# Optimization experiments

Measured on AMD Instinct MI355X. Metric: run time of the kernel, lower is better.

## Reference

```python
import jax, jax.numpy as jnp
import numpy as np


def _gru_layer(x_seq, W_ih, W_hh, b_ih, b_hh):
    # x_seq: [B, T, D_in]; PyTorch gate order: r, z, n
    B, T, _ = x_seq.shape
    H = W_hh.shape[1]
    # Precompute input-to-hidden gates for all timesteps (one big GEMM)
    gx = jnp.einsum('btd,gd->btg', x_seq, W_ih) + b_ih  # [B, T, 3H]

    def step(h, gx_t):
        gh = h @ W_hh.T + b_hh  # [B, 3H]
        r = jax.nn.sigmoid(gx_t[:, :H] + gh[:, :H])
        z = jax.nn.sigmoid(gx_t[:, H:2 * H] + gh[:, H:2 * H])
        n = jnp.tanh(gx_t[:, 2 * H:] + r * gh[:, 2 * H:])
        h_new = (1.0 - z) * n + z * h
        return h_new, h_new

    h0 = jnp.zeros((B, H), dtype=x_seq.dtype)
    _, hs = jax.lax.scan(step, h0, jnp.swapaxes(gx, 0, 1))  # hs: [T, B, H]
    return jnp.swapaxes(hs, 0, 1)  # [B, T, H]


def setup_inputs() -> dict:
    key = jax.random.key(0)
    ks = jax.random.split(key, 11)
    B, T, D, H, O = 64, 512, 128, 512, 1
    s_ih0 = 1.0 / np.sqrt(D)
    s_h = 1.0 / np.sqrt(H)
    return {
        'X': jax.random.normal(ks[0], (B, T, D), dtype=jnp.float32),
        'W_ih0': jax.random.normal(ks[1], (3 * H, D), dtype=jnp.float32) * s_ih0,
        'W_hh0': jax.random.normal(ks[2], (3 * H, H), dtype=jnp.float32) * s_h,
        'b_ih0': jax.random.normal(ks[3], (3 * H,), dtype=jnp.float32) * s_h,
        'b_hh0': jax.random.normal(ks[4], (3 * H,), dtype=jnp.float32) * s_h,
        'W_ih1': jax.random.normal(ks[5], (3 * H, H), dtype=jnp.float32) * s_h,
        'W_hh1': jax.random.normal(ks[6], (3 * H, H), dtype=jnp.float32) * s_h,
        'b_ih1': jax.random.normal(ks[7], (3 * H,), dtype=jnp.float32) * s_h,
        'b_hh1': jax.random.normal(ks[8], (3 * H,), dtype=jnp.float32) * s_h,
        'W_fc': jax.random.normal(ks[9], (O, H), dtype=jnp.float32) * s_h,
        'b_fc': jax.random.normal(ks[10], (O,), dtype=jnp.float32) * s_h,
    }


def reference(X, W_ih0, W_hh0, b_ih0, b_hh0, W_ih1, W_hh1, b_ih1, b_hh1, W_fc, b_fc):
    h1 = _gru_layer(X, W_ih0, W_hh0, b_ih0, b_hh0)     # [B, T, H]
    h2 = _gru_layer(h1, W_ih1, W_hh1, b_ih1, b_hh1)    # [B, T, H]
    out = h2[:, -1, :] @ W_fc.T + b_fc                 # [B, O]
    return out
```

## Files before the change

kernel.cpp:

```cpp
#include <hip/hip_runtime.h>
#include <math.h>

#define B_  64
#define T_  512
#define D0_ 128
#define H_  512
#define G3_ 1536
#define HSTR 512
#define BSTR 528
#define BKg 32
#define SENT 0x7FC00000u

typedef short short8 __attribute__((ext_vector_type(8)));
typedef float f32x4 __attribute__((ext_vector_type(4)));
typedef unsigned uint32x4 __attribute__((ext_vector_type(4)));

__device__ __forceinline__ float fast_sig(float x) {
  return __builtin_amdgcn_rcpf(1.f + __expf(-x));
}
__device__ __forceinline__ float fast_tanh(float x) {
  return 1.f - 2.f * __builtin_amdgcn_rcpf(1.f + __expf(2.f * x));
}

__device__ __forceinline__ unsigned short f2bf_rne(float f) {
  unsigned u = __float_as_uint(f);
  unsigned r = (u + 0x7fffu + ((u >> 16) & 1u)) >> 16;
  return (unsigned short)r;
}
__device__ __forceinline__ float bf2f(unsigned short h) {
  return __uint_as_float(((unsigned)h) << 16);
}

__global__ __launch_bounds__(768, 3) void scan_kernel(
    const unsigned short* __restrict__ WhH, const unsigned short* __restrict__ WhL,
    const float* __restrict__ bhh,
    const float* __restrict__ gx, float* __restrict__ hist,
    int t0, int tc, int gxt0, int gxT)
{
  __shared__ float hsh[4 * HSTR];
  __shared__ unsigned short hbh[4 * BSTR];
  __shared__ unsigned short hbl[4 * BSTR];
  __shared__ float ghp[2][96 * 5];
  __shared__ float bsh[96];

  const int tid = threadIdx.x;
  const int blk = blockIdx.x;
  const int g = blk >> 4, c = blk & 15;
  const int j0 = c << 5;
  const int bbase = g << 2;

  const int wv = tid >> 6, lane = tid & 63;
  const int mtile = wv >> 1, half = wv & 1;
  const int rloc = lane & 15, kq = lane >> 4;
  const int row = mtile * 16 + rloc;
  const int wrow = (row >> 5) * H_ + j0 + (row & 31);

  short8 wh[8], wl[8];
  {
    const unsigned short* RH = WhH + (size_t)wrow * H_ + half * 256 + (kq << 3);
    const unsigned short* RL = WhL + (size_t)wrow * H_ + half * 256 + (kq << 3);
    #pragma unroll
    for (int cc = 0; cc < 8; ++cc) {
      wh[cc] = *(const short8*)(RH + cc * 32);
      wl[cc] = *(const short8*)(RL + cc * 32);
    }
  }
  if (tid < 96)
    bsh[tid] = bhh[(tid >> 5) * H_ + j0 + (tid & 31)];

  size_t go0 = 0;
  if (tid < 128) {
    int bb = tid >> 5, j = tid & 31;
    go0 = ((size_t)(bbase + bb) * gxT) * (size_t)G3_ + j0 + j;
  }
  __syncthreads();

  for (int t = t0; t < t0 + tc; ++t) {
    if (t == 0) {
      for (int idx = tid; idx < 2048; idx += 768) hsh[idx] = 0.f;
      for (int idx = tid; idx < 4 * BSTR; idx += 768) {
        hbh[idx] = 0; hbl[idx] = 0;
      }
    } else if (tid < 512) {
      const int bb = tid >> 7, e4 = tid & 127;
      const unsigned* qp = (const unsigned*)
          (hist + ((size_t)(bbase + bb) * T_ + (t - 1)) * H_) + (e4 << 2);
      uint32x4 v;
      for (;;) {
        asm volatile(
            "global_load_dwordx4 %0, %1, off sc0 sc1\n\t"
            "s_waitcnt vmcnt(0)"
            : "=&v"(v) : "v"(qp) : "memory");
        if (v.x != SENT && v.y != SENT && v.z != SENT && v.w != SENT) break;
      }
      float4 f = make_float4(__uint_as_float(v.x), __uint_as_float(v.y),
                             __uint_as_float(v.z), __uint_as_float(v.w));
      *(float4*)&hsh[bb * HSTR + (e4 << 2)] = f;
      unsigned short h0 = f2bf_rne(f.x), h1 = f2bf_rne(f.y),
                     h2 = f2bf_rne(f.z), h3 = f2bf_rne(f.w);
      *(ushort4*)&hbh[bb * BSTR + (e4 << 2)] = make_ushort4(h0, h1, h2, h3);
      unsigned short l0 = f2bf_rne(f.x - bf2f(h0)), l1 = f2bf_rne(f.y - bf2f(h1)),
                     l2 = f2bf_rne(f.z - bf2f(h2)), l3 = f2bf_rne(f.w - bf2f(h3));
      *(ushort4*)&hbl[bb * BSTR + (e4 << 2)] = make_ushort4(l0, l1, l2, l3);
    }

    float gxr = 0.f, gxz = 0.f, gxn = 0.f;
    if (tid < 128) {
      size_t go = go0 + (size_t)(t - gxt0) * (size_t)G3_;
      gxr = gx[go]; gxz = gx[go + 512]; gxn = gx[go + 1024];
    }
    __syncthreads();

    {
      f32x4 acc = (f32x4){0.f, 0.f, 0.f, 0.f};
      const int bb4 = lane & 3;
      const unsigned short* bhp = hbh + bb4 * BSTR + half * 256 + (kq << 3);
      const unsigned short* blp = hbl + bb4 * BSTR + half * 256 + (kq << 3);
      #pragma unroll
      for (int cc = 0; cc < 8; ++cc) {
        short8 bh = *(const short8*)(bhp + cc * 32);
        short8 bl = *(const short8*)(blp + cc * 32);
        acc = __builtin_amdgcn_mfma_f32_16x16x32_bf16(wh[cc], bh, acc, 0, 0, 0);
        acc = __builtin_amdgcn_mfma_f32_16x16x32_bf16(wh[cc], bl, acc, 0, 0, 0);
        acc = __builtin_amdgcn_mfma_f32_16x16x32_bf16(wl[cc], bh, acc, 0, 0, 0);
        acc = __builtin_amdgcn_mfma_f32_16x16x32_bf16(wl[cc], bl, acc, 0, 0, 0);
      }
      if (rloc < 4) {
        #pragma unroll
        for (int r = 0; r < 4; ++r)
          ghp[half][(mtile * 16 + (kq << 2) + r) * 5 + rloc] = acc[r];
      }
    }
    __syncthreads();

    if (tid < 128) {
      int bb = tid >> 5, j = tid & 31;
      float ghr = ghp[0][ j       * 5 + bb] + ghp[1][ j       * 5 + bb] + bsh[j];
      float ghz = ghp[0][(32 + j) * 5 + bb] + ghp[1][(32 + j) * 5 + bb] + bsh[32 + j];
      float ghn = ghp[0][(64 + j) * 5 + bb] + ghp[1][(64 + j) * 5 + bb] + bsh[64 + j];
      float rg = fast_sig(gxr + ghr);
      float zg = fast_sig(gxz + ghz);
      float ng = fast_tanh(gxn + rg * ghn);
      float hp = hsh[bb * HSTR + j0 + j];
      float hnew = (1.f - zg) * ng + zg * hp;
      __hip_atomic_store(
          (unsigned*)(hist + ((size_t)(bbase + bb) * T_ + t) * H_) + j0 + j,
          __float_as_uint(hnew), __ATOMIC_RELAXED, __HIP_MEMORY_SCOPE_AGENT);
    }
    __syncthreads();
  }
}

__global__ __launch_bounds__(256) void sent_fill(float* hist, int t0, int tc) {
  int i = blockIdx.x * 256 + threadIdx.x;
  int per = tc * (H_ >> 2);
  if (i < B_ * per) {
    int b = i / per, r = i % per;
    uint4* p = (uint4*)(hist + ((size_t)b * T_ + t0) * H_) + r;
    *p = make_uint4(SENT, SENT, SENT, SENT);
  }
}

__global__ __launch_bounds__(256) void conv_split(
    const float* __restrict__ A, int lda, int t0, int tc, int ltc,
    unsigned short* __restrict__ Ah, unsigned short* __restrict__ Al)
{
  int idx = blockIdx.x * 256 + threadIdx.x;
  int m = idx / (lda >> 2), kq = idx % (lda >> 2);
  const float4 v = *(const float4*)
      (A + ((size_t)(m >> ltc) * T_ + t0 + (m & (tc - 1))) * lda + (kq << 2));
  unsigned short h0 = f2bf_rne(v.x), h1 = f2bf_rne(v.y),
                 h2 = f2bf_rne(v.z), h3 = f2bf_rne(v.w);
  unsigned short l0 = f2bf_rne(v.x - bf2f(h0)), l1 = f2bf_rne(v.y - bf2f(h1)),
                 l2 = f2bf_rne(v.z - bf2f(h2)), l3 = f2bf_rne(v.w - bf2f(h3));
  size_t o = (size_t)m * lda + (kq << 2);
  *(ushort4*)(Ah + o) = make_ushort4(h0, h1, h2, h3);
  *(ushort4*)(Al + o) = make_ushort4(l0, l1, l2, l3);
}

__global__ __launch_bounds__(256, 2) void gemm_mfma(
    const unsigned short* __restrict__ Ah, const unsigned short* __restrict__ Al,
    const unsigned short* __restrict__ Bh, const unsigned short* __restrict__ Bl,
    const float* __restrict__ bias, float* __restrict__ gxout, int K)
{
  __shared__ unsigned short sAh[2][128 * BKg], sAl[2][128 * BKg];
  __shared__ unsigned short sBh[2][128 * BKg], sBl[2][128 * BKg];

  const int tid = threadIdx.x;
  const int m0 = blockIdx.x << 7, n0 = blockIdx.y << 7;
  const int wave = tid >> 6, lane = tid & 63;
  const int wr = (wave & 1) << 6, wc = (wave >> 1) << 6;
  const int fm = lane & 15, kh = lane >> 4;

  const int srow = tid >> 2, sq = tid & 3;
  const int lofs0 = srow * BKg + (sq << 3);
  const int lofs1 = (64 + srow) * BKg + (sq << 3);

  f32x4 acc[4][4];
  #pragma unroll
  for (int i = 0; i < 4; ++i)
    #pragma unroll
    for (int j = 0; j < 4; ++j)
      acc[i][j] = (f32x4){0.f, 0.f, 0.f, 0.f};

  float4 pAh[2], pAl[2], pBh[2], pBl[2];
  #define PREFETCH(k0)                                                        \
    {                                                                         \
      size_t a0 = (size_t)(m0 + srow) * K + (k0) + (sq << 3);                 \
      size_t a1 = (size_t)(m0 + 64 + srow) * K + (k0) + (sq << 3);            \
      size_t b0 = (size_t)(n0 + srow) * K + (k0) + (sq << 3);                 \
      size_t b1 = (size_t)(n0 + 64 + srow) * K + (k0) + (sq << 3);            \
      pAh[0] = *(const float4*)&Ah[a0]; pAh[1] = *(const float4*)&Ah[a1];     \
      pAl[0] = *(const float4*)&Al[a0]; pAl[1] = *(const float4*)&Al[a1];     \
      pBh[0] = *(const float4*)&Bh[b0]; pBh[1] = *(const float4*)&Bh[b1];     \
      pBl[0] = *(const float4*)&Bl[b0]; pBl[1] = *(const float4*)&Bl[b1];     \
    }
  #define STORE_LDS(buf)                                                      \
    {                                                                         \
      *(float4*)&sAh[buf][lofs0] = pAh[0]; *(float4*)&sAh[buf][lofs1] = pAh[1];\
      *(float4*)&sAl[buf][lofs0] = pAl[0]; *(float4*)&sAl[buf][lofs1] = pAl[1];\
      *(float4*)&sBh[buf][lofs0] = pBh[0]; *(float4*)&sBh[buf][lofs1] = pBh[1];\
      *(float4*)&sBl[buf][lofs0] = pBl[0]; *(float4*)&sBl[buf][lofs1] = pBl[1];\
    }

  PREFETCH(0);
  STORE_LDS(0);
  int buf = 0;

  for (int k0 = 0; k0 < K; k0 += BKg) {
    __syncthreads();
    const bool more = (k0 + BKg) < K;
    if (more) PREFETCH(k0 + BKg);

    short8 fAh[4], fAl[4], fBh[4], fBl[4];
    #pragma unroll
    for (int i = 0; i < 4; ++i) {
      int ao = (wr + i * 16 + fm) * BKg + (kh << 3);
      int bo = (wc + i * 16 + fm) * BKg + (kh << 3);
      fAh[i] = *(const short8*)&sAh[buf][ao];
      fAl[i] = *(const short8*)&sAl[buf][ao];
      fBh[i] = *(const short8*)&sBh[buf][bo];
      fBl[i] = *(const short8*)&sBl[buf][bo];
    }
    #pragma unroll
    for (int i = 0; i < 4; ++i)
      #pragma unroll
      for (int j = 0; j < 4; ++j) {
        acc[i][j] = __builtin_amdgcn_mfma_f32_16x16x32_bf16(
            fAh[i], fBh[j], acc[i][j], 0, 0, 0);
        acc[i][j] = __builtin_amdgcn_mfma_f32_16x16x32_bf16(
            fAh[i], fBl[j], acc[i][j], 0, 0, 0);
        acc[i][j] = __builtin_amdgcn_mfma_f32_16x16x32_bf16(
            fAl[i], fBh[j], acc[i][j], 0, 0, 0);
      }
    if (more) {
      STORE_LDS(buf ^ 1);
      buf ^= 1;
    }
  }

  #pragma unroll
  for (int j = 0; j < 4; ++j) {
    int col = n0 + wc + j * 16 + fm;
    float bv = bias[col];
    #pragma unroll
    for (int i = 0; i < 4; ++i) {
      int rowb = m0 + wr + i * 16 + (kh << 2);
      #pragma unroll
      for (int r = 0; r < 4; ++r)
        gxout[(size_t)(rowb + r) * G3_ + col] = acc[i][j][r] + bv;
    }
  }
}

__global__ void fc_kernel(const float* __restrict__ hist, const float* __restrict__ Wfc,
                          const float* __restrict__ bfc, float* __restrict__ out)
{
  int b = blockIdx.x, lane = threadIdx.x;
  const float* h = hist + ((size_t)b*T_ + (T_-1))*H_;
  float acc = 0.f;
  for (int j = lane; j < H_; j += 64) acc += h[j]*Wfc[j];
  #pragma unroll
  for (int off = 32; off; off >>= 1) acc += __shfl_down(acc, off, 64);
  if (lane == 0) out[b] = acc + bfc[0];
}

extern "C" void kernel_launch(void* const* d_in, const int* in_sizes, int n_in,
                              void* d_out, int out_size, void* d_ws, size_t ws_size,
                              hipStream_t stream)
{
  const float* X    = (const float*)d_in[0];
  const float* Wih0 = (const float*)d_in[1];
  const float* Whh0 = (const float*)d_in[2];
  const float* bih0 = (const float*)d_in[3];
  const float* bhh0 = (const float*)d_in[4];
  const float* Wih1 = (const float*)d_in[5];
  const float* Whh1 = (const float*)d_in[6];
  const float* bih1 = (const float*)d_in[7];
  const float* bhh1 = (const float*)d_in[8];
  const float* Wfc  = (const float*)d_in[9];
  const float* bfc  = (const float*)d_in[10];

  float* hist = (float*)((char*)d_ws + 4096);
  const size_t histB = (size_t)B_*T_*H_*4;

  const size_t bB = (size_t)G3_ * 512 * 2;
  const size_t wB = (size_t)G3_ * H_ * 2;
  int tcg = 128;
  {
    size_t fixed = 4096 + histB + 2 * bB + 2 * wB;
    if      (ws_size >= fixed + (size_t)B_*512*((size_t)G3_*4 + 512*4)) tcg = 512;
    else if (ws_size >= fixed + (size_t)B_*256*((size_t)G3_*4 + 512*4)) tcg = 256;
  }
  int ltc = 31 - __builtin_clz((unsigned)tcg);

  float* gxbuf = (float*)((char*)d_ws + 4096 + histB);
  const size_t gxB = (size_t)B_*tcg*G3_*4;
  unsigned short* Ahb = (unsigned short*)((char*)gxbuf + gxB);
  const size_t aB = (size_t)B_*tcg*512*2;
  unsigned short* Alb = (unsigned short*)((char*)Ahb + aB);
  unsigned short* Bhb = (unsigned short*)((char*)Alb + aB);
  unsigned short* Blb = (unsigned short*)((char*)Bhb + bB);
  unsigned short* Whb = (unsigned short*)((char*)Blb + bB);
  unsigned short* Wlb = (unsigned short*)((char*)Whb + wB);

  const int sentGridFull = (B_ * T_ * (H_ >> 2) + 255) / 256;
  const int sentGridChunk = (B_ * tcg * (H_ >> 2) + 255) / 256;

  hipLaunchKernelGGL(sent_fill, dim3(sentGridFull), dim3(256), 0, stream,
                     hist, 0, T_);

  for (int lay = 0; lay < 2; ++lay) {
    const float* A   = lay ? (const float*)hist : X;
    int lda          = lay ? H_ : D0_;
    const float* Wih = lay ? Wih1 : Wih0;
    const float* bih = lay ? bih1 : bih0;
    const float* Whh = lay ? Whh1 : Whh0;
    const float* bhh = lay ? bhh1 : bhh0;

    hipLaunchKernelGGL(conv_split, dim3((G3_*lda/4)/256), dim3(256), 0, stream,
                       Wih, lda, 0, 1 << 30, 30, Bhb, Blb);
    hipLaunchKernelGGL(conv_split, dim3((G3_*H_/4)/256), dim3(256), 0, stream,
                       Whh, H_, 0, 1 << 30, 30, Whb, Wlb);

    for (int t0g = 0; t0g < T_; t0g += tcg) {
      int M = B_ * tcg;
      hipLaunchKernelGGL(conv_split, dim3((M*lda/4)/256), dim3(256), 0, stream,
                         A, lda, t0g, tcg, ltc, Ahb, Alb);
      if (lay == 1)
        hipLaunchKernelGGL(sent_fill, dim3(sentGridChunk), dim3(256), 0, stream,
                           hist, t0g, tcg);
      dim3 ggrid(M >> 7, G3_ >> 7);
      hipLaunchKernelGGL(gemm_mfma, ggrid, dim3(256), 0, stream,
                         Ahb, Alb, Bhb, Blb, bih, gxbuf, lda);
      hipLaunchKernelGGL(scan_kernel, dim3(256), dim3(768), 0, stream,
                         Whb, Wlb, bhh, (const float*)gxbuf, hist,
                         t0g, tcg, t0g, tcg);
    }
  }

  hipLaunchKernelGGL(fc_kernel, dim3(64), dim3(64), 0, stream,
                     (const float*)hist, Wfc, bfc, (float*)d_out);
}
```

Measured before the change: 2.711 ms.

## Split K four ways, interleave two M-tiles with independent accumulators, drop lo*lo MFMA

Each wave now covers two 16-row M tiles over a quarter of K instead of one M tile over half of K. It keeps six independent MFMA accumulators per wave so there is no serial dependent chain, and it drops the low*low bf16 correction term. This shortens the per-step MFMA dependency chain in the latency-bound recurrent scan, at the cost of more LDS partial sums (four partials summed per gate) and a small loss of precision from removing the lo*lo product.

```diff
diff --git a/kernel.cpp b/kernel.cpp
--- a/kernel.cpp
+++ b/kernel.cpp
@@ -40,7 +40,7 @@
   __shared__ float hsh[4 * HSTR];
   __shared__ unsigned short hbh[4 * BSTR];
   __shared__ unsigned short hbl[4 * BSTR];
-  __shared__ float ghp[2][96 * 5];
+  __shared__ float ghp[4][96 * 5];
   __shared__ float bsh[96];
 
   const int tid = threadIdx.x;
@@ -50,19 +50,25 @@
   const int bbase = g << 2;
 
   const int wv = tid >> 6, lane = tid & 63;
-  const int mtile = wv >> 1, half = wv & 1;
+  const int q = wv & 3, p = wv >> 2;
   const int rloc = lane & 15, kq = lane >> 4;
-  const int row = mtile * 16 + rloc;
-  const int wrow = (row >> 5) * H_ + j0 + (row & 31);
-
-  short8 wh[8], wl[8];
+  const int rowA = 32 * p + rloc;
+  const int rowB = 32 * p + 16 + rloc;
+  const int wrowA = (rowA >> 5) * H_ + j0 + (rowA & 31);
+  const int wrowB = (rowB >> 5) * H_ + j0 + (rowB & 31);
+
+  short8 whA[4], wlA[4], whB[4], wlB[4];
   {
-    const unsigned short* RH = WhH + (size_t)wrow * H_ + half * 256 + (kq << 3);
-    const unsigned short* RL = WhL + (size_t)wrow * H_ + half * 256 + (kq << 3);
-    #pragma unroll
-    for (int cc = 0; cc < 8; ++cc) {
-      wh[cc] = *(const short8*)(RH + cc * 32);
-      wl[cc] = *(const short8*)(RL + cc * 32);
+    const unsigned short* RHA = WhH + (size_t)wrowA * H_ + q * 128 + (kq << 3);
+    const unsigned short* RLA = WhL + (size_t)wrowA * H_ + q * 128 + (kq << 3);
+    const unsigned short* RHB = WhH + (size_t)wrowB * H_ + q * 128 + (kq << 3);
+    const unsigned short* RLB = WhL + (size_t)wrowB * H_ + q * 128 + (kq << 3);
+    #pragma unroll
+    for (int cc = 0; cc < 4; ++cc) {
+      whA[cc] = *(const short8*)(RHA + cc * 32);
+      wlA[cc] = *(const short8*)(RLA + cc * 32);
+      whB[cc] = *(const short8*)(RHB + cc * 32);
+      wlB[cc] = *(const short8*)(RLB + cc * 32);
     }
   }
   if (tid < 96)
@@ -112,32 +118,43 @@
     __syncthreads();
 
     {
-      f32x4 acc = (f32x4){0.f, 0.f, 0.f, 0.f};
+      f32x4 aHHA = (f32x4){0.f,0.f,0.f,0.f}, aHLA = aHHA, aLHA = aHHA;
+      f32x4 aHHB = aHHA, aHLB = aHHA, aLHB = aHHA;
       const int bb4 = lane & 3;
-      const unsigned short* bhp = hbh + bb4 * BSTR + half * 256 + (kq << 3);
-      const unsigned short* blp = hbl + bb4 * BSTR + half * 256 + (kq << 3);
+      const unsigned short* bhp = hbh + bb4 * BSTR + q * 128 + (kq << 3);
+      const unsigned short* blp = hbl + bb4 * BSTR + q * 128 + (kq << 3);
       #pragma unroll
-      for (int cc = 0; cc < 8; ++cc) {
+      for (int cc = 0; cc < 4; ++cc) {
         short8 bh = *(const short8*)(bhp + cc * 32);
         short8 bl = *(const short8*)(blp + cc * 32);
-        acc = __builtin_amdgcn_mfma_f32_16x16x32_bf16(wh[cc], bh, acc, 0, 0, 0);
-        acc = __builtin_amdgcn_mfma_f32_16x16x32_bf16(wh[cc], bl, acc, 0, 0, 0);
-        acc = __builtin_amdgcn_mfma_f32_16x16x32_bf16(wl[cc], bh, acc, 0, 0, 0);
-        acc = __builtin_amdgcn_mfma_f32_16x16x32_bf16(wl[cc], bl, acc, 0, 0, 0);
-      }
+        aHHA = __builtin_amdgcn_mfma_f32_16x16x32_bf16(whA[cc], bh, aHHA, 0, 0, 0);
+        aHHB = __builtin_amdgcn_mfma_f32_16x16x32_bf16(whB[cc], bh, aHHB, 0, 0, 0);
+        aHLA = __builtin_amdgcn_mfma_f32_16x16x32_bf16(whA[cc], bl, aHLA, 0, 0, 0);
+        aHLB = __builtin_amdgcn_mfma_f32_16x16x32_bf16(whB[cc], bl, aHLB, 0, 0, 0);
+        aLHA = __builtin_amdgcn_mfma_f32_16x16x32_bf16(wlA[cc], bh, aLHA, 0, 0, 0);
+        aLHB = __builtin_amdgcn_mfma_f32_16x16x32_bf16(wlB[cc], bh, aLHB, 0, 0, 0);
+      }
+      f32x4 accA = (aHHA + aHLA) + aLHA;
+      f32x4 accB = (aHHB + aHLB) + aLHB;
       if (rloc < 4) {
         #pragma unroll
         for (int r = 0; r < 4; ++r)
-          ghp[half][(mtile * 16 + (kq << 2) + r) * 5 + rloc] = acc[r];
+          ghp[q][((2 * p) * 16 + (kq << 2) + r) * 5 + rloc] = accA[r];
+        #pragma unroll
+        for (int r = 0; r < 4; ++r)
+          ghp[q][((2 * p + 1) * 16 + (kq << 2) + r) * 5 + rloc] = accB[r];
       }
     }
     __syncthreads();
 
     if (tid < 128) {
       int bb = tid >> 5, j = tid & 31;
-      float ghr = ghp[0][ j       * 5 + bb] + ghp[1][ j       * 5 + bb] + bsh[j];
-      float ghz = ghp[0][(32 + j) * 5 + bb] + ghp[1][(32 + j) * 5 + bb] + bsh[32 + j];
-      float ghn = ghp[0][(64 + j) * 5 + bb] + ghp[1][(64 + j) * 5 + bb] + bsh[64 + j];
+      float ghr = (ghp[0][ j       * 5 + bb] + ghp[1][ j       * 5 + bb]) +
+                  (ghp[2][ j       * 5 + bb] + ghp[3][ j       * 5 + bb]) + bsh[j];
+      float ghz = (ghp[0][(32 + j) * 5 + bb] + ghp[1][(32 + j) * 5 + bb]) +
+                  (ghp[2][(32 + j) * 5 + bb] + ghp[3][(32 + j) * 5 + bb]) + bsh[32 + j];
+      float ghn = (ghp[0][(64 + j) * 5 + bb] + ghp[1][(64 + j) * 5 + bb]) +
+                  (ghp[2][(64 + j) * 5 + bb] + ghp[3][(64 + j) * 5 + bb]) + bsh[64 + j];
       float rg = fast_sig(gxr + ghr);
       float zg = fast_sig(gxz + ghz);
       float ng = fast_tanh(gxn + rg * ghn);
```

Result: faster. 2.596 ms (-4.2%).
